# Optimization experiments

Measured on AMD Instinct MI355X. Metric: run time of the kernel, lower is better.

## Reference

```python
import jax, jax.numpy as jnp
import numpy as np

NX, DX, H, DO = 8192, 8, 1024, 1


def setup_inputs() -> dict:
    key = jax.random.key(0)
    ks = jax.random.split(key, 7)
    s1 = 1.0 / np.sqrt(DX)  # torch Linear default init bound
    s2 = 1.0 / np.sqrt(H)
    x = jax.random.normal(ks[0], (NX, DX), jnp.float32)
    W1 = jax.random.uniform(ks[1], (H, DX), jnp.float32, -s1, s1)
    b1 = jax.random.uniform(ks[2], (H,), jnp.float32, -s1, s1)
    W2 = jax.random.uniform(ks[3], (H, H), jnp.float32, -s2, s2)
    b2 = jax.random.uniform(ks[4], (H,), jnp.float32, -s2, s2)
    W3 = jax.random.uniform(ks[5], (DO, H), jnp.float32, -s2, s2)
    b3 = jax.random.uniform(ks[6], (DO,), jnp.float32, -s2, s2)
    return {"x": x, "W1": W1, "b1": b1, "W2": W2, "b2": b2, "W3": W3, "b3": b3}


def reference(x, W1, b1, W2, b2, W3, b3):
    # Forward: Linear -> Tanh -> Linear -> Tanh -> Linear
    z1 = jnp.tanh(x @ W1.T + b1)          # [nx, h]
    z2 = jnp.tanh(z1 @ W2.T + b2)         # [nx, h]
    y = z2 @ W3.T + b3                    # [nx, out]

    # DerivTanh(h) = 4/(e^-h + e^h)^2 = sech^2(h) = 1 - tanh(h)^2
    d1 = 1.0 - z1 * z1                    # [nx, h]
    d2 = 1.0 - z2 * z2                    # [nx, h]

    # Vectorized analytic Jacobian (original loops over each input dim k):
    # tmp_k = d2 * (W2 @ (d1 * W1[:, k]))  then  dydx_k = W3 @ tmp_k
    J = d1[:, :, None] * W1[None, :, :]                    # [nx, h, dx]
    J = d2[:, :, None] * jnp.einsum('ij,njk->nik', W2, J)  # [nx, h, dx]
    dydx = jnp.einsum('oj,njk->nok', W3, J)                # [nx, out, dx]
    # Match original list-of-dx ordering: dydx[k] has shape [nx, out]
    dydx = jnp.transpose(dydx, (2, 0, 1))                  # [dx, nx, out]
    return y, dydx
```

## Files before the change

kernel.cpp:

```cpp
#include <hip/hip_runtime.h>
#include <stdint.h>

#define NXS 8192
#define HS  1024

typedef __attribute__((ext_vector_type(8))) short short8;
typedef __attribute__((ext_vector_type(4))) float f32x4;

__device__ __forceinline__ float bf2f(uint32_t b) {
    union { uint32_t u; float f; } c; c.u = b << 16; return c.f;
}
__device__ __forceinline__ uint16_t f2bf(float f) {
    union { float f; uint32_t u; } c; c.f = f;
    return (uint16_t)((c.u + 0x7fffu + ((c.u >> 16) & 1u)) >> 16);
}
__device__ __forceinline__ float fast_tanh(float x) {
    float xc = fminf(fmaxf(x, -15.f), 15.f);
    return 1.f - __fdividef(2.f, __expf(2.f * xc) + 1.f);
}
__device__ __forceinline__ void async_cp16(const void* g, void* l) {
    __builtin_amdgcn_global_load_lds(
        (const __attribute__((address_space(1))) void*)g,
        (__attribute__((address_space(3))) void*)l,
        16, 0, 0);
}

__global__ __launch_bounds__(256) void k01(
    const float* __restrict__ x, const float* __restrict__ W1,
    const float* __restrict__ b1, const float* __restrict__ W2,
    const float* __restrict__ b3, uint16_t* __restrict__ Z1,
    uint16_t* __restrict__ Bp1, uint16_t* __restrict__ Bp2,
    uint16_t* __restrict__ W1T, float* __restrict__ out)
{
    __shared__ float xs[8][8];
    const int b = blockIdx.x, t = threadIdx.x;
    if (b < 1024) {
        const int n0 = b * 8;
        if (t < 64) xs[t >> 3][t & 7] = x[n0 * 8 + t];
        const int j = t * 4;
        float w[4][8];
#pragma unroll
        for (int c = 0; c < 4; ++c) {
            float4 w0 = *(const float4*)(W1 + (j + c) * 8);
            float4 w1 = *(const float4*)(W1 + (j + c) * 8 + 4);
            w[c][0] = w0.x; w[c][1] = w0.y; w[c][2] = w0.z; w[c][3] = w0.w;
            w[c][4] = w1.x; w[c][5] = w1.y; w[c][6] = w1.z; w[c][7] = w1.w;
        }
        float4 bb = *(const float4*)(b1 + j);
        const float bv[4] = {bb.x, bb.y, bb.z, bb.w};
        __syncthreads();
#pragma unroll
        for (int s = 0; s < 8; ++s) {
            ushort4 o;
            uint16_t* op = (uint16_t*)&o;
#pragma unroll
            for (int c = 0; c < 4; ++c) {
                float sum = bv[c];
#pragma unroll
                for (int k = 0; k < 8; ++k) sum += xs[s][k] * w[c][k];
                op[c] = f2bf(fast_tanh(sum));
            }
            *(ushort4*)(Z1 + (size_t)(n0 + s) * HS + j) = o;
        }
    } else if (b < 1536) {
        const int tid = (b - 1024) * 256 + t;
        const int l = tid & 63, c = (tid >> 6) & 31, g = tid >> 11;
        const int lr = l & 15, lq = l >> 4;
        const float* src = W2 + (size_t)(g * 16 + lr) * HS + c * 32 + lq * 8;
        float4 a0 = *(const float4*)src;
        float4 a1 = *(const float4*)(src + 4);
        uint16_t o[8];
        o[0] = f2bf(a0.x); o[1] = f2bf(a0.y); o[2] = f2bf(a0.z); o[3] = f2bf(a0.w);
        o[4] = f2bf(a1.x); o[5] = f2bf(a1.y); o[6] = f2bf(a1.z); o[7] = f2bf(a1.w);
        *(ushort4*)(Bp1 + (size_t)tid * 8)     = *(ushort4*)&o[0];
        *(ushort4*)(Bp1 + (size_t)tid * 8 + 4) = *(ushort4*)&o[4];
    } else if (b < 2048) {
        const int tid = (b - 1536) * 256 + t;
        const int l = tid & 63, c = (tid >> 6) & 31, g = tid >> 11;
        const int lr = l & 15, lq = l >> 4;
        uint16_t o[8];
#pragma unroll
        for (int j2 = 0; j2 < 8; ++j2)
            o[j2] = f2bf(W2[(size_t)(c * 32 + lq * 8 + j2) * HS + g * 16 + lr]);
        *(ushort4*)(Bp2 + (size_t)tid * 8)     = *(ushort4*)&o[0];
        *(ushort4*)(Bp2 + (size_t)tid * 8 + 4) = *(ushort4*)&o[4];
    } else if (b < 2336) {
        const int idx = (b - 2048) * 256 + t;
        out[idx] = (idx < NXS) ? b3[0] : 0.f;
    } else {
        const int idx = (b - 2336) * 256 + t;
        const int r = idx >> 10, cc = idx & 1023;
        W1T[idx] = (r < 8) ? f2bf(W1[cc * 8 + r]) : (uint16_t)0;
    }
}

template <int MODE>
__global__ __launch_bounds__(256, 4) void gemm_k(
    const uint16_t* __restrict__ A, const uint16_t* __restrict__ Bp,
    const float* __restrict__ bias, const float* __restrict__ W3,
    uint16_t* __restrict__ Out, float* __restrict__ yOut,
    const uint16_t* __restrict__ Z1, const uint16_t* __restrict__ W1T,
    float* __restrict__ dOut)
{
    __shared__ __attribute__((aligned(16))) uint16_t smem[12288];
    const int t = threadIdx.x;
    const int wave = t >> 6, lane = t & 63;
    const int lq = lane >> 4, lr = lane & 15;
    const int rowBase = blockIdx.x * 64;
    const int colBase = blockIdx.y * 128;

    const uint16_t* gA;
    {
        int rA = t >> 2, q = (t & 3) ^ ((rA >> 1) & 3);
        gA = A + (size_t)(rowBase + rA) * HS + q * 8;
    }
    const uint16_t* gB0;
    const uint16_t* gB1;
    {
        int s0 = t, s1 = t + 256;
        gB0 = Bp + ((size_t)(colBase >> 4) + (s0 >> 6)) * 16384 + (size_t)(s0 & 63) * 8;
        gB1 = Bp + ((size_t)(colBase >> 4) + (s1 >> 6)) * 16384 + (size_t)(s1 & 63) * 8;
    }

    f32x4 acc[4][2] = {};

    async_cp16(gA,  (char*)smem + t * 16);
    async_cp16(gB0, (char*)smem + 4096 + t * 16);
    async_cp16(gB1, (char*)smem + 8192 + t * 16);
    __syncthreads();

    int buf = 0;
    for (int c = 0; c < 32; ++c) {
        if (c < 31) {
            char* d = (char*)smem + (buf ^ 1) * 12288;
            async_cp16(gA + (c + 1) * 32,        d + t * 16);
            async_cp16(gB0 + (size_t)(c + 1) * 512, d + 4096 + t * 16);
            async_cp16(gB1 + (size_t)(c + 1) * 512, d + 8192 + t * 16);
        }
        const uint16_t* pA = smem + buf * 6144;
        const uint16_t* pB = pA + 2048;
        short8 bfrag[2];
#pragma unroll
        for (int tj = 0; tj < 2; ++tj)
            bfrag[tj] = *(const short8*)(pB + (((wave << 1) + tj) * 64 + lane) * 8);
        short8 af[4];
#pragma unroll
        for (int ti = 0; ti < 4; ++ti) {
            int ar = ti * 16 + lr;
            af[ti] = *(const short8*)(pA + ar * 32
                      + ((lq ^ ((ar >> 1) & 3)) << 3));
        }
#pragma unroll
        for (int ti = 0; ti < 4; ++ti)
#pragma unroll
            for (int tj = 0; tj < 2; ++tj)
                acc[ti][tj] = __builtin_amdgcn_mfma_f32_16x16x32_bf16(
                    af[ti], bfrag[tj], acc[ti][tj], 0, 0, 0);
        __syncthreads();
        buf ^= 1;
    }

    if (MODE == 0) {
        float cB[2], cW[2]; int cCol[2];
#pragma unroll
        for (int tj = 0; tj < 2; ++tj) {
            cCol[tj] = colBase + wave * 32 + tj * 16 + lr;
            cB[tj] = bias[cCol[tj]];
            cW[tj] = W3[cCol[tj]];
        }
#pragma unroll
        for (int ti = 0; ti < 4; ++ti) {
#pragma unroll
            for (int r = 0; r < 4; ++r) {
                int row = rowBase + ti * 16 + lq * 4 + r;
                float ys = 0.f;
#pragma unroll
                for (int tj = 0; tj < 2; ++tj) {
                    float z2 = fast_tanh(acc[ti][tj][r] + cB[tj]);
                    ys += z2 * cW[tj];
                    Out[(size_t)row * HS + cCol[tj]] = f2bf((1.f - z2 * z2) * cW[tj]);
                }
                ys += __shfl_xor(ys, 1); ys += __shfl_xor(ys, 2);
                ys += __shfl_xor(ys, 4); ys += __shfl_xor(ys, 8);
                if (lr == 0) atomicAdd(&yOut[row], ys);
            }
        }
    } else {
#pragma unroll
        for (int ti = 0; ti < 4; ++ti)
#pragma unroll
            for (int r = 0; r < 4; ++r) {
                int rowl = ti * 16 + lq * 4 + r;
                const size_t zrow = (size_t)(rowBase + rowl) * HS + colBase;
#pragma unroll
                for (int tj = 0; tj < 2; ++tj) {
                    int coll = wave * 32 + tj * 16 + lr;
                    float z1 = bf2f(Z1[zrow + coll]);
                    smem[rowl * 136 + coll] =
                        f2bf(acc[ti][tj][r] * (1.f - z1 * z1));
                }
            }
        __syncthreads();
        f32x4 dd = {};
#pragma unroll
        for (int kb = 0; kb < 4; ++kb) {
            short8 aF = *(const short8*)(smem + (wave * 16 + lr) * 136
                                         + kb * 32 + lq * 8);
            short8 bF = *(const short8*)(W1T + (size_t)lr * HS + colBase
                                         + kb * 32 + lq * 8);
            dd = __builtin_amdgcn_mfma_f32_16x16x32_bf16(aF, bF, dd, 0, 0, 0);
        }
        if (lr < 8) {
            int row = rowBase + wave * 16 + lq * 4;
#pragma unroll
            for (int rg = 0; rg < 4; ++rg)
                atomicAdd(&dOut[(size_t)lr * NXS + row + rg], dd[rg]);
        }
    }
}

extern "C" void kernel_launch(void* const* d_in, const int* in_sizes, int n_in,
                              void* d_out, int out_size, void* d_ws, size_t ws_size,
                              hipStream_t stream) {
    (void)in_sizes; (void)n_in; (void)out_size; (void)ws_size;
    const float* x  = (const float*)d_in[0];
    const float* W1 = (const float*)d_in[1];
    const float* b1 = (const float*)d_in[2];
    const float* W2 = (const float*)d_in[3];
    const float* b2 = (const float*)d_in[4];
    const float* W3 = (const float*)d_in[5];
    const float* b3 = (const float*)d_in[6];
    float* out = (float*)d_out;

    char* ws = (char*)d_ws;
    uint16_t* Z1  = (uint16_t*)(ws);
    uint16_t* V   = (uint16_t*)(ws + (size_t)16 * 1024 * 1024);
    uint16_t* Bp1 = (uint16_t*)(ws + (size_t)32 * 1024 * 1024);
    uint16_t* Bp2 = (uint16_t*)(ws + (size_t)34 * 1024 * 1024);
    uint16_t* W1T = (uint16_t*)(ws + (size_t)36 * 1024 * 1024);

    k01<<<2400, 256, 0, stream>>>(x, W1, b1, W2, b3, Z1, Bp1, Bp2, W1T, out);
    gemm_k<0><<<dim3(NXS / 64, HS / 128), 256, 0, stream>>>(
        Z1, Bp1, b2, W3, V, out, nullptr, nullptr, nullptr);
    gemm_k<1><<<dim3(NXS / 64, HS / 128), 256, 0, stream>>>(
        V, Bp2, nullptr, nullptr, nullptr, nullptr, Z1, W1T, out + NXS);
}
```

Baseline: 133.9 us.

## Triple-buffer GEMM LDS pipeline with partial vmcnt waits

Moves the GEMM main loop from double to triple buffering in LDS, prefetching two K-chunks ahead. It replaces the full __syncthreads drain with s_waitcnt vmcnt(3) plus a raw barrier, so one chunk's loads stay in flight across iterations. LDS use grows from 24KB to 36KB per block, which may lower occupancy under launch_bounds(256,4). The hand-written waitcnt also assumes the compiler issues no other vector memory ops inside the loop.

```diff
diff --git a/kernel.cpp b/kernel.cpp
--- a/kernel.cpp
+++ b/kernel.cpp
@@ -102,7 +102,7 @@
     const uint16_t* __restrict__ Z1, const uint16_t* __restrict__ W1T,
     float* __restrict__ dOut)
 {
-    __shared__ __attribute__((aligned(16))) uint16_t smem[12288];
+    __shared__ __attribute__((aligned(16))) uint16_t smem[18432];
     const int t = threadIdx.x;
     const int wave = t >> 6, lane = t & 63;
     const int lq = lane >> 4, lr = lane & 15;
@@ -121,23 +121,35 @@
         gB0 = Bp + ((size_t)(colBase >> 4) + (s0 >> 6)) * 16384 + (size_t)(s0 & 63) * 8;
         gB1 = Bp + ((size_t)(colBase >> 4) + (s1 >> 6)) * 16384 + (size_t)(s1 & 63) * 8;
     }
+    const int ldsA  = t * 16;
+    const int ldsB0 = 4096 + t * 16;
+    const int ldsB1 = 8192 + t * 16;
 
     f32x4 acc[4][2] = {};
 
-    async_cp16(gA,  (char*)smem + t * 16);
-    async_cp16(gB0, (char*)smem + 4096 + t * 16);
-    async_cp16(gB1, (char*)smem + 8192 + t * 16);
-    __syncthreads();
-
-    int buf = 0;
+    async_cp16(gA,         (char*)smem + ldsA);
+    async_cp16(gB0,        (char*)smem + ldsB0);
+    async_cp16(gB1,        (char*)smem + ldsB1);
+    async_cp16(gA + 32,    (char*)smem + 12288 + ldsA);
+    async_cp16(gB0 + 512,  (char*)smem + 12288 + ldsB0);
+    async_cp16(gB1 + 512,  (char*)smem + 12288 + ldsB1);
+    gA += 64; gB0 += 1024; gB1 += 1024;
+    asm volatile("s_waitcnt vmcnt(3)" ::: "memory");
+    __builtin_amdgcn_s_barrier();
+
+    int rb = 0;
+    int wb = 2;
+#pragma unroll 1
     for (int c = 0; c < 32; ++c) {
-        if (c < 31) {
-            char* d = (char*)smem + (buf ^ 1) * 12288;
-            async_cp16(gA + (c + 1) * 32,        d + t * 16);
-            async_cp16(gB0 + (size_t)(c + 1) * 512, d + 4096 + t * 16);
-            async_cp16(gB1 + (size_t)(c + 1) * 512, d + 8192 + t * 16);
-        }
-        const uint16_t* pA = smem + buf * 6144;
+        if (c < 30) {
+            char* d = (char*)smem + wb * 12288;
+            async_cp16(gA,  d + ldsA);
+            async_cp16(gB0, d + ldsB0);
+            async_cp16(gB1, d + ldsB1);
+            gA += 32; gB0 += 512; gB1 += 512;
+            asm volatile("" ::: "memory");
+        }
+        const uint16_t* pA = smem + rb * 6144;
         const uint16_t* pB = pA + 2048;
         short8 bfrag[2];
 #pragma unroll
@@ -156,8 +168,14 @@
             for (int tj = 0; tj < 2; ++tj)
                 acc[ti][tj] = __builtin_amdgcn_mfma_f32_16x16x32_bf16(
                     af[ti], bfrag[tj], acc[ti][tj], 0, 0, 0);
-        __syncthreads();
-        buf ^= 1;
+        if (c < 30) {
+            asm volatile("s_waitcnt vmcnt(3)" ::: "memory");
+        } else {
+            asm volatile("s_waitcnt vmcnt(0)" ::: "memory");
+        }
+        __builtin_amdgcn_s_barrier();
+        rb = (rb == 2) ? 0 : rb + 1;
+        wb = (wb == 2) ? 0 : wb + 1;
     }
 
     if (MODE == 0) {
```

Result: slower. 137.1 us (+2.4%).

## Fuse three launches into one cooperative persistent kernel with grid syncs

Applied to the files above, without the earlier changes.

Merges the prep kernel and both GEMM kernels into a single cooperative persistent kernel. Blocks loop over the former block indices, and grid.sync separates the three phases. The aim is to remove kernel launch gaps and inter-kernel drain. The trade-offs are grid-sync cost, a grid capped at occupancy-limited size (up to 1024 blocks, so tiles may be processed in rounds), and extra __syncthreads for shared-memory reuse across iterations. It falls back to the three separate launches if the cooperative launch fails.

```diff
diff --git a/kernel.cpp b/kernel.cpp
--- a/kernel.cpp
+++ b/kernel.cpp
@@ -1,5 +1,8 @@
 #include <hip/hip_runtime.h>
+#include <hip/hip_cooperative_groups.h>
 #include <stdint.h>
+
+namespace cg = cooperative_groups;
 
 #define NXS 8192
 #define HS  1024
@@ -25,18 +28,18 @@
         16, 0, 0);
 }
 
-__global__ __launch_bounds__(256) void k01(
+__device__ __forceinline__ void k01_body(int b, int t,
     const float* __restrict__ x, const float* __restrict__ W1,
     const float* __restrict__ b1, const float* __restrict__ W2,
     const float* __restrict__ b3, uint16_t* __restrict__ Z1,
     uint16_t* __restrict__ Bp1, uint16_t* __restrict__ Bp2,
-    uint16_t* __restrict__ W1T, float* __restrict__ out)
-{
-    __shared__ float xs[8][8];
-    const int b = blockIdx.x, t = threadIdx.x;
+    uint16_t* __restrict__ W1T, float* __restrict__ out,
+    uint16_t* smem)
+{
     if (b < 1024) {
+        float* xs = (float*)smem;
         const int n0 = b * 8;
-        if (t < 64) xs[t >> 3][t & 7] = x[n0 * 8 + t];
+        if (t < 64) xs[t] = x[n0 * 8 + t];
         const int j = t * 4;
         float w[4][8];
 #pragma unroll
@@ -57,11 +60,12 @@
             for (int c = 0; c < 4; ++c) {
                 float sum = bv[c];
 #pragma unroll
-                for (int k = 0; k < 8; ++k) sum += xs[s][k] * w[c][k];
+                for (int k = 0; k < 8; ++k) sum += xs[s * 8 + k] * w[c][k];
                 op[c] = f2bf(fast_tanh(sum));
             }
             *(ushort4*)(Z1 + (size_t)(n0 + s) * HS + j) = o;
         }
+        __syncthreads();
     } else if (b < 1536) {
         const int tid = (b - 1024) * 256 + t;
         const int l = tid & 63, c = (tid >> 6) & 31, g = tid >> 11;
@@ -95,19 +99,17 @@
 }
 
 template <int MODE>
-__global__ __launch_bounds__(256, 4) void gemm_k(
+__device__ __forceinline__ void gemm_tile(int bx, int by, int t,
     const uint16_t* __restrict__ A, const uint16_t* __restrict__ Bp,
     const float* __restrict__ bias, const float* __restrict__ W3,
     uint16_t* __restrict__ Out, float* __restrict__ yOut,
-    const uint16_t* __restrict__ Z1, const uint16_t* __restrict__ W1T,
-    float* __restrict__ dOut)
-{
-    __shared__ __attribute__((aligned(16))) uint16_t smem[12288];
-    const int t = threadIdx.x;
+    const uint16_t* __restrict__ Z1c, const uint16_t* __restrict__ W1T,
+    float* __restrict__ dOut, uint16_t* smem)
+{
     const int wave = t >> 6, lane = t & 63;
     const int lq = lane >> 4, lr = lane & 15;
-    const int rowBase = blockIdx.x * 64;
-    const int colBase = blockIdx.y * 128;
+    const int rowBase = bx * 64;
+    const int colBase = by * 128;
 
     const uint16_t* gA;
     {
@@ -133,7 +135,7 @@
     for (int c = 0; c < 32; ++c) {
         if (c < 31) {
             char* d = (char*)smem + (buf ^ 1) * 12288;
-            async_cp16(gA + (c + 1) * 32,        d + t * 16);
+            async_cp16(gA + (c + 1) * 32,           d + t * 16);
             async_cp16(gB0 + (size_t)(c + 1) * 512, d + 4096 + t * 16);
             async_cp16(gB1 + (size_t)(c + 1) * 512, d + 8192 + t * 16);
         }
@@ -185,6 +187,7 @@
                 if (lr == 0) atomicAdd(&yOut[row], ys);
             }
         }
+        __syncthreads();
     } else {
 #pragma unroll
         for (int ti = 0; ti < 4; ++ti)
@@ -195,7 +198,7 @@
 #pragma unroll
                 for (int tj = 0; tj < 2; ++tj) {
                     int coll = wave * 32 + tj * 16 + lr;
-                    float z1 = bf2f(Z1[zrow + coll]);
+                    float z1 = bf2f(Z1c[zrow + coll]);
                     smem[rowl * 136 + coll] =
                         f2bf(acc[ti][tj][r] * (1.f - z1 * z1));
                 }
@@ -216,7 +219,62 @@
             for (int rg = 0; rg < 4; ++rg)
                 atomicAdd(&dOut[(size_t)lr * NXS + row + rg], dd[rg]);
         }
-    }
+        __syncthreads();
+    }
+}
+
+__global__ __launch_bounds__(256, 4) void mega(
+    const float* __restrict__ x,  const float* __restrict__ W1,
+    const float* __restrict__ b1, const float* __restrict__ W2,
+    const float* __restrict__ b2, const float* __restrict__ W3,
+    const float* __restrict__ b3, uint16_t* __restrict__ Z1,
+    uint16_t* __restrict__ Bp1, uint16_t* __restrict__ Bp2,
+    uint16_t* __restrict__ W1T, uint16_t* __restrict__ V,
+    float* __restrict__ outY, float* __restrict__ outD)
+{
+    __shared__ __attribute__((aligned(16))) uint16_t smem[12288];
+    const int t = threadIdx.x;
+    cg::grid_group grid = cg::this_grid();
+
+    for (int b = blockIdx.x; b < 2400; b += gridDim.x)
+        k01_body(b, t, x, W1, b1, W2, b3, Z1, Bp1, Bp2, W1T, outY, smem);
+    __threadfence();
+    grid.sync();
+
+    for (int bid = blockIdx.x; bid < 1024; bid += gridDim.x)
+        gemm_tile<0>(bid & 127, bid >> 7, t, Z1, Bp1, b2, W3, V, outY,
+                     nullptr, nullptr, nullptr, smem);
+    __threadfence();
+    grid.sync();
+
+    for (int bid = blockIdx.x; bid < 1024; bid += gridDim.x)
+        gemm_tile<1>(bid & 127, bid >> 7, t, V, Bp2, nullptr, nullptr,
+                     nullptr, nullptr, Z1, W1T, outD, smem);
+}
+
+__global__ __launch_bounds__(256) void k01(
+    const float* __restrict__ x, const float* __restrict__ W1,
+    const float* __restrict__ b1, const float* __restrict__ W2,
+    const float* __restrict__ b3, uint16_t* __restrict__ Z1,
+    uint16_t* __restrict__ Bp1, uint16_t* __restrict__ Bp2,
+    uint16_t* __restrict__ W1T, float* __restrict__ out)
+{
+    __shared__ __attribute__((aligned(16))) uint16_t smem[128];
+    k01_body(blockIdx.x, threadIdx.x, x, W1, b1, W2, b3, Z1, Bp1, Bp2, W1T,
+             out, smem);
+}
+
+template <int MODE>
+__global__ __launch_bounds__(256, 4) void gemm_k(
+    const uint16_t* __restrict__ A, const uint16_t* __restrict__ Bp,
+    const float* __restrict__ bias, const float* __restrict__ W3,
+    uint16_t* __restrict__ Out, float* __restrict__ yOut,
+    const uint16_t* __restrict__ Z1, const uint16_t* __restrict__ W1T,
+    float* __restrict__ dOut)
+{
+    __shared__ __attribute__((aligned(16))) uint16_t smem[12288];
+    gemm_tile<MODE>(blockIdx.x, blockIdx.y, threadIdx.x, A, Bp, bias, W3,
+                    Out, yOut, Z1, W1T, dOut, smem);
 }
 
 extern "C" void kernel_launch(void* const* d_in, const int* in_sizes, int n_in,
@@ -238,10 +296,38 @@
     uint16_t* Bp1 = (uint16_t*)(ws + (size_t)32 * 1024 * 1024);
     uint16_t* Bp2 = (uint16_t*)(ws + (size_t)34 * 1024 * 1024);
     uint16_t* W1T = (uint16_t*)(ws + (size_t)36 * 1024 * 1024);
-
-    k01<<<2400, 256, 0, stream>>>(x, W1, b1, W2, b3, Z1, Bp1, Bp2, W1T, out);
-    gemm_k<0><<<dim3(NXS / 64, HS / 128), 256, 0, stream>>>(
-        Z1, Bp1, b2, W3, V, out, nullptr, nullptr, nullptr);
-    gemm_k<1><<<dim3(NXS / 64, HS / 128), 256, 0, stream>>>(
-        V, Bp2, nullptr, nullptr, nullptr, nullptr, Z1, W1T, out + NXS);
-}
+    float* outY = out;
+    float* outD = out + NXS;
+
+    static int coopGrid = -2;
+    if (coopGrid == -2) {
+        int per = 0;
+        hipError_t qe = hipOccupancyMaxActiveBlocksPerMultiprocessor(
+            &per, mega, 256, 0);
+        if (qe == hipSuccess && per > 0) {
+            int g = per * 256;
+            coopGrid = g < 1024 ? g : 1024;
+        } else {
+            coopGrid = -1;
+        }
+    }
+
+    bool coopDone = false;
+    if (coopGrid > 0) {
+        void* args[14] = {
+            (void*)&x, (void*)&W1, (void*)&b1, (void*)&W2, (void*)&b2,
+            (void*)&W3, (void*)&b3, (void*)&Z1, (void*)&Bp1, (void*)&Bp2,
+            (void*)&W1T, (void*)&V, (void*)&outY, (void*)&outD };
+        hipError_t e = hipLaunchCooperativeKernel(
+            mega, dim3(coopGrid), dim3(256), args, 0, stream);
+        coopDone = (e == hipSuccess);
+    }
+
+    if (!coopDone) {
+        k01<<<2400, 256, 0, stream>>>(x, W1, b1, W2, b3, Z1, Bp1, Bp2, W1T, out);
+        gemm_k<0><<<dim3(NXS / 64, HS / 128), 256, 0, stream>>>(
+            Z1, Bp1, b2, W3, V, outY, nullptr, nullptr, nullptr);
+        gemm_k<1><<<dim3(NXS / 64, HS / 128), 256, 0, stream>>>(
+            V, Bp2, nullptr, nullptr, nullptr, nullptr, Z1, W1T, outD);
+    }
+}
```

Result: slower. 393.8 us (+194.1%).
